# Optimization experiments

Hardware: AMD Instinct MI355X
Metric: run time of the kernel (lower is better)

Reference implementation:

```python
import jax, jax.numpy as jnp
import numpy as np
import math

N_PATHS = 2048
N_STEPS = 512
N_FWD = 40
N_FACTORS = 3
H = 0.1
ALPHA = H - 0.5            # fBM kernel exponent
BETA_SABR = 0.5
SHIFT = 0.02
DT = 1.0 / N_STEPS
GAMMA_CONST = math.gamma(H + 0.5)
BETA_DECAY = 0.05


def setup_inputs() -> dict:
    key = jax.random.key(0)
    tenors = np.linspace(0.0, 10.0, N_FWD + 1)
    T = tenors[:-1]
    tau = np.diff(tenors).astype(np.float32)
    F0 = np.full(N_FWD, 0.02, dtype=np.float32)
    # alphas = base normal vols / |F0+shift|^beta  (as in __init__)
    base_vols = np.full(N_FWD, 0.006)
    eta_F0 = np.abs(F0 + SHIFT) ** BETA_SABR
    alphas = (base_vols / eta_F0).astype(np.float32)
    rhos = np.full(N_FWD, -0.3, dtype=np.float32)
    nus = np.full(N_FWD, 0.5, dtype=np.float32)
    # PCA loadings from exponential spatial correlation (as in __init__)
    corr = np.exp(-BETA_DECAY * np.abs(T[:, None] - T[None, :]))
    evals, evecs = np.linalg.eigh(corr)
    idx = np.argsort(evals)[::-1][:N_FACTORS]
    L = evecs[:, idx] * np.sqrt(np.clip(evals[idx], 0.0, None))[None, :]
    L = L / np.sqrt((L ** 2).sum(axis=1, keepdims=True))
    Lam = np.triu(L @ L.T, 1).astype(np.float32)
    # Brownian increments, pre-scaled by sqrt(dt) (replaces Sobol+icdf draw)
    dz = jax.random.normal(key, (N_PATHS, N_STEPS, N_FACTORS + 1), dtype=jnp.float32) * float(np.sqrt(DT))
    return {
        "dz_all": dz,
        "F0": jnp.asarray(F0),
        "alphas": jnp.asarray(alphas),
        "rhos": jnp.asarray(rhos),
        "nus": jnp.asarray(nus),
        "tau": jnp.asarray(tau),
        "loadings": jnp.asarray(L.astype(np.float32)),
        "Lambda_upper": jnp.asarray(Lam),
    }


def reference(dz_all, F0, alphas, rhos, nus, tau, loadings, Lambda_upper):
    n_paths, n_steps, _ = dz_all.shape
    dtype = dz_all.dtype
    # --- hybrid-scheme Volterra / fBM kernel [n_steps, n_steps] ---
    idx = jnp.arange(n_steps)
    k = jnp.maximum(idx[:, None] - idx[None, :] + 1, 0).astype(dtype)
    # with b_eval='optimal', riemann == exact weights, so the where(k<=kappa) is identity
    exact_w = (k ** (ALPHA + 1.0) - jnp.maximum(k - 1.0, 0.0) ** (ALPHA + 1.0)) / (ALPHA + 1.0)
    kernel = jnp.where(idx[:, None] >= idx[None, :], exact_w * (DT ** ALPHA) / GAMMA_CONST, 0.0)
    # variance compensator [N, n_steps]
    var_comp = 0.5 * (nus ** 2)[:, None] * jnp.sum(kernel ** 2, axis=1)[None, :] * DT
    # --- correlated Brownian drivers and fBM via kernel convolution ---
    wr = jnp.einsum('psf,nf->psn', dz_all[..., :N_FACTORS], loadings)          # [P,S,N]
    fbm4 = jnp.einsum('ts,psd->ptd', kernel, dz_all)                            # [P,S,4]
    fbm_curve = jnp.einsum('ptf,nf->ptn', fbm4[..., :N_FACTORS], loadings)      # [P,S,N]
    fbm = rhos * fbm_curve + jnp.sqrt(1.0 - rhos ** 2) * fbm4[..., -1:]
    unit_vols = jnp.exp(nus * fbm - var_comp.T[None])                            # [P,S,N]
    v2_dt = unit_vols ** 2 * DT
    # --- frozen-drift forward dynamics ---
    eta_f0 = jnp.abs(F0 + SHIFT) ** BETA_SABR
    vol_scale = alphas * eta_f0
    omega_0 = tau * vol_scale / (1.0 + tau * F0)
    mu_0 = -vol_scale * (Lambda_upper @ omega_0)
    dF = mu_0 * v2_dt + wr * (unit_vols * vol_scale)
    F_path = F0 + jnp.cumsum(dF, axis=1)                                         # [P,S,N]
    return jnp.concatenate([jnp.broadcast_to(F0, (n_paths, 1, F0.shape[0])), F_path], axis=1)
```

## Files before the change

kernel.cpp:

```cpp
#include <hip/hip_runtime.h>
#include <math.h>

#define NS 512
#define NF 40
#define ROWS_OUT 513
#define DTC (1.0f / 512.0f)
#define PLANE 520


__global__ __launch_bounds__(64) void const_kernel(
    const float* __restrict__ F0, const float* __restrict__ alphas,
    const float* __restrict__ rhos, const float* __restrict__ nus,
    const float* __restrict__ tau, const float* __restrict__ L,
    const float* __restrict__ Lam, float* __restrict__ ws)
{
    __shared__ float omega0[NF];
    __shared__ float vs_s[NF];
    int n = threadIdx.x;
    if (n < NF) {
        float f0 = F0[n];
        float vs = alphas[n] * sqrtf(fabsf(f0 + 0.02f));
        vs_s[n] = vs;
        omega0[n] = tau[n] * vs / (1.0f + tau[n] * f0);
    }
    __syncthreads();
    if (n < NF) {
        float s = 0.0f;
        for (int j = 0; j < NF; ++j) s += Lam[n * NF + j] * omega0[j];
        float vs = vs_s[n];
        float mu0 = -vs * s;
        float rho = rhos[n], nu = nus[n];
        float* c = ws + 1024 + n * 8;
        c[0] = vs * L[n * 3 + 0];
        c[1] = vs * L[n * 3 + 1];
        c[2] = vs * L[n * 3 + 2];
        c[3] = nu * rho / fmaxf(vs, 1e-30f);
        c[4] = nu * sqrtf(fmaxf(1.0f - rho * rho, 0.0f));
        c[5] = 0.5f * nu * nu * DTC;
        c[6] = mu0 * DTC;
        c[7] = F0[n];
    }
}

template<int CTRL, int RM>
__device__ __forceinline__ float dpp_add(float v) {
    int t = __builtin_amdgcn_update_dpp(0, __float_as_int(v), CTRL, RM, 0xf, true);
    return v + __int_as_float(t);
}
__device__ __forceinline__ float wave_iscan(float v) {
    v = dpp_add<0x111, 0xf>(v);
    v = dpp_add<0x112, 0xf>(v);
    v = dpp_add<0x114, 0xf>(v);
    v = dpp_add<0x118, 0xf>(v);
    v = dpp_add<0x142, 0xa>(v);
    v = dpp_add<0x143, 0xc>(v);
    return v;
}

__device__ __forceinline__ void fma4(float4& acc, float c, const float4& v) {
    acc.x = fmaf(c, v.x, acc.x);
    acc.y = fmaf(c, v.y, acc.y);
    acc.z = fmaf(c, v.z, acc.z);
    acc.w = fmaf(c, v.w, acc.w);
}

__global__ __launch_bounds__(256, 4) void path_kernel(
    const float* __restrict__ dz, const float* __restrict__ ws,
    float* __restrict__ out)
{
    __shared__ float planes[2 * 4 * PLANE];
    __shared__ float wp[768];
    __shared__ float cw2[NS];
    __shared__ float chunk[64 * 41];

    int tid = threadIdx.x;
    int lane = tid & 63;
    int wv = __builtin_amdgcn_readfirstlane(tid >> 6);
    int pA = blockIdx.x * 2, pB = pA + 1;
    const float4* dzgA = (const float4*)dz + (size_t)pA * NS;
    const float4* dzgB = (const float4*)dz + (size_t)pB * NS;

    for (int i = tid; i < 768; i += 256) wp[i] = (i < 256) ? 0.0f : ws[i - 256];
    for (int i = tid; i < NS; i += 256) cw2[i] = ws[NS + i];
    __syncthreads();

    {
        int path = wv >> 1;
        int half = wv & 1;
        int i = half * 64 + lane;
        int gmax = half ? 128 : 64;
        const float4* dzg = path ? dzgB : dzgA;
        float* pf = planes + path * 4 * PLANE;
        const float4* wp4 = (const float4*)wp;
        float4 a0 = make_float4(0.f, 0.f, 0.f, 0.f);
        float4 a1 = a0, a2 = a0, a3 = a0;
        #pragma unroll 2
        for (int g = 0; g < gmax; ++g) {
            float4 d0 = dzg[4 * g + 0];
            float4 d1 = dzg[4 * g + 1];
            float4 d2 = dzg[4 * g + 2];
            float4 d3 = dzg[4 * g + 3];
            float4 lo = wp4[63 + i - g];
            float4 hi = wp4[64 + i - g];
            fma4(a0, hi.x, d0); fma4(a1, hi.y, d0); fma4(a2, hi.z, d0); fma4(a3, hi.w, d0);
            fma4(a0, lo.w, d1); fma4(a1, hi.x, d1); fma4(a2, hi.y, d1); fma4(a3, hi.z, d1);
            fma4(a0, lo.z, d2); fma4(a1, lo.w, d2); fma4(a2, hi.x, d2); fma4(a3, hi.y, d2);
            fma4(a0, lo.y, d3); fma4(a1, lo.z, d3); fma4(a2, lo.w, d3); fma4(a3, hi.x, d3);
        }
        ((float4*)(pf + 0 * PLANE))[i] = make_float4(a0.x, a1.x, a2.x, a3.x);
        ((float4*)(pf + 1 * PLANE))[i] = make_float4(a0.y, a1.y, a2.y, a3.y);
        ((float4*)(pf + 2 * PLANE))[i] = make_float4(a0.z, a1.z, a2.z, a3.z);
        ((float4*)(pf + 3 * PLANE))[i] = make_float4(a0.w, a1.w, a2.w, a3.w);
    }

    float carryA[10], carryB[10];
    #pragma unroll
    for (int j = 0; j < 10; ++j) { carryA[j] = 0.0f; carryB[j] = 0.0f; }

    float* outA = out + (size_t)pA * (ROWS_OUT * NF);
    float* outB = out + (size_t)pB * (ROWS_OUT * NF);
    if (tid < NF) outA[tid] = ws[1024 + tid * 8 + 7];
    if (tid >= 64 && tid < 64 + NF) outB[tid - 64] = ws[1024 + (tid - 64) * 8 + 7];

    __syncthreads();

    for (int cix = 0; cix < 8; ++cix) {
        int t = cix * 64 + lane;
        float cw = cw2[t];
        #pragma unroll
        for (int path = 0; path < 2; ++path) {
            const float* pf = planes + path * 4 * PLANE;
            float fx = pf[t], fy = pf[PLANE + t], fz = pf[2 * PLANE + t], fw = pf[3 * PLANE + t];
            float4 d = path ? dzgB[t] : dzgA[t];
            float* carry = path ? carryB : carryA;
            #pragma unroll
            for (int j = 0; j < 10; ++j) {
                int n = wv * 10 + j;
                const float* c = ws + 1024 + n * 8;
                float cC0 = c[0], cC1 = c[1], cC2 = c[2], q = c[3];
                float cA3 = c[4], ca = c[5], cm0 = c[6], f0 = c[7];
                float dotf = fx * cC0 + fy * cC1 + fz * cC2;
                float arg = fmaf(q, dotf, fmaf(cA3, fw, -ca * cw));
                float uv = __expf(arg);
                float dotc = d.x * cC0 + d.y * cC1 + d.z * cC2;
                float dF = uv * fmaf(cm0, uv, dotc);
                float v = wave_iscan(dF) + carry[j];
                carry[j] = __int_as_float(__builtin_amdgcn_readlane(__float_as_int(v), 63));
                chunk[lane * 41 + n] = v + f0;
            }
            __syncthreads();
            float* o = (path ? outB : outA) + NF + cix * (64 * NF);
            #pragma unroll
            for (int k = 0; k < 10; ++k) {
                int f = tid + k * 256;
                __builtin_nontemporal_store(chunk[f + f / 40], o + f);
            }
            __syncthreads();
        }
    }
}

extern "C" void kernel_launch(void* const* d_in, const int* in_sizes, int n_in,
                              void* d_out, int out_size, void* d_ws, size_t ws_size,
                              hipStream_t stream) {
    const float* dz   = (const float*)d_in[0];
    const float* F0   = (const float*)d_in[1];
    const float* alph = (const float*)d_in[2];
    const float* rhos = (const float*)d_in[3];
    const float* nus  = (const float*)d_in[4];
    const float* tau  = (const float*)d_in[5];
    const float* L    = (const float*)d_in[6];
    const float* Lam  = (const float*)d_in[7];
    float* ws = (float*)d_ws;
    float* out = (float*)d_out;

    int n_paths = in_sizes[0] / (NS * 4);

    static float h_w[1024];
    {
        const double g06 = 1.4891922488128171;
        double dta = pow(512.0, 0.4);
        double acc = 0.0;
        for (int m = 0; m < 512; ++m) {
            double wv = (pow((double)m + 1.0, 0.6) - pow((double)m, 0.6)) * (1.0 / 0.6) * dta / g06;
            h_w[m] = (float)wv;
            acc += wv * wv;
            h_w[512 + m] = (float)acc;
        }
    }
    hipMemcpyAsync(ws, h_w, sizeof(h_w), hipMemcpyHostToDevice, stream);

    const_kernel<<<1, 64, 0, stream>>>(F0, alph, rhos, nus, tau, L, Lam, ws);
    path_kernel<<<n_paths / 2, 256, 0, stream>>>(dz, ws, out);
}
```

Measured before the change: 263.1 us.

## Balance convolution work across waves and compute kernel weights on device

The convolution phase previously gave the second-half wave twice the work (128 vs 64 groups). Now the first wave also computes the g<32 partial contributions for the upper rows and stores them in a shared partial buffer, so each wave does about 96 groups. Those partials are added back when reading the planes for the second half of the time steps. Separately, the fBM kernel weights and their cumulative squares are now computed in const_kernel on the GPU instead of on the host plus an H2D memcpy. The cost is extra shared memory and a serial 512-step prefix on one thread.

```diff
diff --git a/kernel.cpp b/kernel.cpp
--- a/kernel.cpp
+++ b/kernel.cpp
@@ -6,6 +6,7 @@
 #define ROWS_OUT 513
 #define DTC (1.0f / 512.0f)
 #define PLANE 520
+#define PPL 260
 
 
 __global__ __launch_bounds__(64) void const_kernel(
@@ -14,9 +15,22 @@
     const float* __restrict__ tau, const float* __restrict__ L,
     const float* __restrict__ Lam, float* __restrict__ ws)
 {
+    __shared__ double wd[NS];
     __shared__ float omega0[NF];
     __shared__ float vs_s[NF];
     int n = threadIdx.x;
+
+    {
+        const double g06 = 1.4891922488128171;
+        const double dta = pow(512.0, 0.4);
+        #pragma unroll
+        for (int k = 0; k < 8; ++k) {
+            int m = n * 8 + k;
+            double wv = (pow((double)m + 1.0, 0.6) - pow((double)m, 0.6)) * (1.0 / 0.6) * dta / g06;
+            wd[m] = wv;
+            ws[m] = (float)wv;
+        }
+    }
     if (n < NF) {
         float f0 = F0[n];
         float vs = alphas[n] * sqrtf(fabsf(f0 + 0.02f));
@@ -24,6 +38,10 @@
         omega0[n] = tau[n] * vs / (1.0f + tau[n] * f0);
     }
     __syncthreads();
+    if (n == 0) {
+        double acc = 0.0;
+        for (int m = 0; m < NS; ++m) { acc += wd[m] * wd[m]; ws[NS + m] = (float)acc; }
+    }
     if (n < NF) {
         float s = 0.0f;
         for (int j = 0; j < NF; ++j) s += Lam[n * NF + j] * omega0[j];
@@ -64,11 +82,18 @@
     acc.w = fmaf(c, v.w, acc.w);
 }
 
+#define CONV_STEP(A0, A1, A2, A3, LO, HI)                                          \
+    fma4(A0, HI.x, d0); fma4(A1, HI.y, d0); fma4(A2, HI.z, d0); fma4(A3, HI.w, d0);\
+    fma4(A0, LO.w, d1); fma4(A1, HI.x, d1); fma4(A2, HI.y, d1); fma4(A3, HI.z, d1);\
+    fma4(A0, LO.z, d2); fma4(A1, LO.w, d2); fma4(A2, HI.x, d2); fma4(A3, HI.y, d2);\
+    fma4(A0, LO.y, d3); fma4(A1, LO.z, d3); fma4(A2, LO.w, d3); fma4(A3, HI.x, d3);
+
 __global__ __launch_bounds__(256, 4) void path_kernel(
     const float* __restrict__ dz, const float* __restrict__ ws,
     float* __restrict__ out)
 {
     __shared__ float planes[2 * 4 * PLANE];
+    __shared__ float partial[2 * 4 * PPL];
     __shared__ float wp[768];
     __shared__ float cw2[NS];
     __shared__ float chunk[64 * 41];
@@ -87,30 +112,60 @@
     {
         int path = wv >> 1;
         int half = wv & 1;
-        int i = half * 64 + lane;
-        int gmax = half ? 128 : 64;
         const float4* dzg = path ? dzgB : dzgA;
         float* pf = planes + path * 4 * PLANE;
+        float* pp = partial + path * 4 * PPL;
         const float4* wp4 = (const float4*)wp;
-        float4 a0 = make_float4(0.f, 0.f, 0.f, 0.f);
-        float4 a1 = a0, a2 = a0, a3 = a0;
-        #pragma unroll 2
-        for (int g = 0; g < gmax; ++g) {
-            float4 d0 = dzg[4 * g + 0];
-            float4 d1 = dzg[4 * g + 1];
-            float4 d2 = dzg[4 * g + 2];
-            float4 d3 = dzg[4 * g + 3];
-            float4 lo = wp4[63 + i - g];
-            float4 hi = wp4[64 + i - g];
-            fma4(a0, hi.x, d0); fma4(a1, hi.y, d0); fma4(a2, hi.z, d0); fma4(a3, hi.w, d0);
-            fma4(a0, lo.w, d1); fma4(a1, hi.x, d1); fma4(a2, hi.y, d1); fma4(a3, hi.z, d1);
-            fma4(a0, lo.z, d2); fma4(a1, lo.w, d2); fma4(a2, hi.x, d2); fma4(a3, hi.y, d2);
-            fma4(a0, lo.y, d3); fma4(a1, lo.z, d3); fma4(a2, lo.w, d3); fma4(a3, hi.x, d3);
+        float4 z4 = make_float4(0.f, 0.f, 0.f, 0.f);
+        if (half == 0) {
+            int i = lane;
+            float4 a0 = z4, a1 = z4, a2 = z4, a3 = z4;
+            float4 b0 = z4, b1 = z4, b2 = z4, b3 = z4;
+            #pragma unroll 2
+            for (int g = 0; g < 32; ++g) {
+                float4 d0 = dzg[4 * g + 0];
+                float4 d1 = dzg[4 * g + 1];
+                float4 d2 = dzg[4 * g + 2];
+                float4 d3 = dzg[4 * g + 3];
+                float4 lo = wp4[63 + i - g], hi = wp4[64 + i - g];
+                CONV_STEP(a0, a1, a2, a3, lo, hi)
+                float4 lo2 = wp4[127 + i - g], hi2 = wp4[128 + i - g];
+                CONV_STEP(b0, b1, b2, b3, lo2, hi2)
+            }
+            #pragma unroll 2
+            for (int g = 32; g < 64; ++g) {
+                float4 d0 = dzg[4 * g + 0];
+                float4 d1 = dzg[4 * g + 1];
+                float4 d2 = dzg[4 * g + 2];
+                float4 d3 = dzg[4 * g + 3];
+                float4 lo = wp4[63 + i - g], hi = wp4[64 + i - g];
+                CONV_STEP(a0, a1, a2, a3, lo, hi)
+            }
+            ((float4*)(pf + 0 * PLANE))[i] = make_float4(a0.x, a1.x, a2.x, a3.x);
+            ((float4*)(pf + 1 * PLANE))[i] = make_float4(a0.y, a1.y, a2.y, a3.y);
+            ((float4*)(pf + 2 * PLANE))[i] = make_float4(a0.z, a1.z, a2.z, a3.z);
+            ((float4*)(pf + 3 * PLANE))[i] = make_float4(a0.w, a1.w, a2.w, a3.w);
+            ((float4*)(pp + 0 * PPL))[lane] = make_float4(b0.x, b1.x, b2.x, b3.x);
+            ((float4*)(pp + 1 * PPL))[lane] = make_float4(b0.y, b1.y, b2.y, b3.y);
+            ((float4*)(pp + 2 * PPL))[lane] = make_float4(b0.z, b1.z, b2.z, b3.z);
+            ((float4*)(pp + 3 * PPL))[lane] = make_float4(b0.w, b1.w, b2.w, b3.w);
+        } else {
+            int i = 64 + lane;
+            float4 a0 = z4, a1 = z4, a2 = z4, a3 = z4;
+            #pragma unroll 2
+            for (int g = 32; g < 128; ++g) {
+                float4 d0 = dzg[4 * g + 0];
+                float4 d1 = dzg[4 * g + 1];
+                float4 d2 = dzg[4 * g + 2];
+                float4 d3 = dzg[4 * g + 3];
+                float4 lo = wp4[63 + i - g], hi = wp4[64 + i - g];
+                CONV_STEP(a0, a1, a2, a3, lo, hi)
+            }
+            ((float4*)(pf + 0 * PLANE))[i] = make_float4(a0.x, a1.x, a2.x, a3.x);
+            ((float4*)(pf + 1 * PLANE))[i] = make_float4(a0.y, a1.y, a2.y, a3.y);
+            ((float4*)(pf + 2 * PLANE))[i] = make_float4(a0.z, a1.z, a2.z, a3.z);
+            ((float4*)(pf + 3 * PLANE))[i] = make_float4(a0.w, a1.w, a2.w, a3.w);
         }
-        ((float4*)(pf + 0 * PLANE))[i] = make_float4(a0.x, a1.x, a2.x, a3.x);
-        ((float4*)(pf + 1 * PLANE))[i] = make_float4(a0.y, a1.y, a2.y, a3.y);
-        ((float4*)(pf + 2 * PLANE))[i] = make_float4(a0.z, a1.z, a2.z, a3.z);
-        ((float4*)(pf + 3 * PLANE))[i] = make_float4(a0.w, a1.w, a2.w, a3.w);
     }
 
     float carryA[10], carryB[10];
@@ -131,6 +186,14 @@
         for (int path = 0; path < 2; ++path) {
             const float* pf = planes + path * 4 * PLANE;
             float fx = pf[t], fy = pf[PLANE + t], fz = pf[2 * PLANE + t], fw = pf[3 * PLANE + t];
+            if (cix >= 4) {
+                const float* pp = partial + path * 4 * PPL;
+                int tt = t - 256;
+                fx += pp[tt];
+                fy += pp[PPL + tt];
+                fz += pp[2 * PPL + tt];
+                fw += pp[3 * PPL + tt];
+            }
             float4 d = path ? dzgB[t] : dzgA[t];
             float* carry = path ? carryB : carryA;
             #pragma unroll
@@ -176,20 +239,6 @@
 
     int n_paths = in_sizes[0] / (NS * 4);
 
-    static float h_w[1024];
-    {
-        const double g06 = 1.4891922488128171;
-        double dta = pow(512.0, 0.4);
-        double acc = 0.0;
-        for (int m = 0; m < 512; ++m) {
-            double wv = (pow((double)m + 1.0, 0.6) - pow((double)m, 0.6)) * (1.0 / 0.6) * dta / g06;
-            h_w[m] = (float)wv;
-            acc += wv * wv;
-            h_w[512 + m] = (float)acc;
-        }
-    }
-    hipMemcpyAsync(ws, h_w, sizeof(h_w), hipMemcpyHostToDevice, stream);
-
     const_kernel<<<1, 64, 0, stream>>>(F0, alph, rhos, nus, tau, L, Lam, ws);
     path_kernel<<<n_paths / 2, 256, 0, stream>>>(dz, ws, out);
 }
```

Result: slower. 273.9 us (+4.1%).
